# Performance work log

Measured on AMD Instinct MI355X. Metric: run time of the kernel, lower is better.

## Reference

```python
import jax, jax.numpy as jnp
import numpy as np

DIM = 2
WIDTH = 128
N = 262144
T = 101
W0 = 44.0


def setup_inputs() -> dict:
    key = jax.random.key(0)
    ks = jax.random.split(key, 7)
    # time grid: arange scaled to [0, 1] (dt = 0.01)
    t = jnp.arange(T, dtype=jnp.float32) / (T - 1)
    x0 = jax.random.normal(ks[0], (N, DIM), dtype=jnp.float32)
    # SIREN init: first layer U(-1/dim, 1/dim); later layers U(-sqrt(6/fan_in)/w0, +)
    c0 = 1.0 / DIM
    ch = float(np.sqrt(6.0 / WIDTH) / W0)
    W1 = jax.random.uniform(ks[1], (DIM, WIDTH), jnp.float32, -c0, c0)
    b1 = jax.random.uniform(ks[2], (WIDTH,), jnp.float32, -c0, c0)
    W2 = jax.random.uniform(ks[3], (WIDTH, WIDTH), jnp.float32, -ch, ch)
    b2 = jax.random.uniform(ks[4], (WIDTH,), jnp.float32, -ch, ch)
    W3 = jax.random.uniform(ks[5], (WIDTH, DIM), jnp.float32, -ch, ch)
    b3 = jax.random.uniform(ks[6], (DIM,), jnp.float32, -ch, ch)
    return {"t": t, "x0": x0, "W1": W1, "b1": b1, "W2": W2, "b2": b2, "W3": W3, "b3": b3}


def reference(t, x0, W1, b1, W2, b2, W3, b3):
    def f(x):
        h = jnp.sin(W0 * (x @ W1 + b1))   # [N, WIDTH]
        h = jnp.sin(W0 * (h @ W2 + b2))   # [N, WIDTH]
        return h @ W3 + b3                # [N, DIM]

    # torchdiffeq fixed-grid 'rk4' uses the 3/8-rule (rk4_alt_step_func)
    def step(y, dt):
        k1 = f(y)
        k2 = f(y + dt * k1 / 3.0)
        k3 = f(y + dt * (k2 - k1 / 3.0))
        k4 = f(y + dt * (k1 - k2 + k3))
        y1 = y + (k1 + 3.0 * (k2 + k3) + k4) * dt * 0.125
        return y1, y1

    dts = t[1:] - t[:-1]                  # [T-1]
    _, ys = jax.lax.scan(step, x0, dts)   # [T-1, N, DIM]
    return jnp.concatenate([x0[None], ys], axis=0)  # [T, N, DIM]
```

## Files before the change

### kernel.cpp

```cpp
#include <hip/hip_runtime.h>


#define W0F    44.0f
#define INV2PI 0.15915494309189535f
#define SCALE  (W0F * INV2PI)
#define WIDTH  128
#define NPART  262144
#define TSTEPS 101

typedef short s16x8 __attribute__((ext_vector_type(8)));
typedef float f32x4 __attribute__((ext_vector_type(4)));

__device__ __forceinline__ float sin_rev(float z) {
    return __builtin_amdgcn_sinf(z);
}
__device__ __forceinline__ unsigned short f2bf(float x) {
    __bf16 b = (__bf16)x;
    return __builtin_bit_cast(unsigned short, b);
}
__device__ __forceinline__ float bf2f(unsigned short u) {
    unsigned int v = ((unsigned int)u) << 16;
    return __builtin_bit_cast(float, v);
}
__device__ __forceinline__ float trunc16f(float v) {
    return __builtin_bit_cast(float, __builtin_bit_cast(unsigned int, v) & 0xffff0000u);
}
__device__ __forceinline__ unsigned int pack_hi16(float vlo, float vhi) {
    return __builtin_amdgcn_perm(__builtin_bit_cast(unsigned int, vhi),
                                 __builtin_bit_cast(unsigned int, vlo),
                                 0x07060302u);
}

#define ROR_ADD(x, ctrl) ((x) + __builtin_bit_cast(float, \
    __builtin_amdgcn_update_dpp(0, __builtin_bit_cast(int, (x)), (ctrl), 0xF, 0xF, false)))
__device__ __forceinline__ float row_sum16(float x) {
    x = ROR_ADD(x, 0x128);
    x = ROR_ADD(x, 0x124);
    x = ROR_ADD(x, 0x122);
    x = ROR_ADD(x, 0x121);
    return x;
}

__device__ __forceinline__ float sel16(const float g[16], int idx) {
    float a[8], b[4], c[2];
    #pragma unroll
    for (int i = 0; i < 8; ++i) a[i] = (idx & 8) ? g[i + 8] : g[i];
    #pragma unroll
    for (int i = 0; i < 4; ++i) b[i] = (idx & 4) ? a[i + 4] : a[i];
    #pragma unroll
    for (int i = 0; i < 2; ++i) c[i] = (idx & 2) ? b[i + 2] : b[i];
    return (idx & 1) ? c[1] : c[0];
}

__global__ void prep_kernel(const float* __restrict__ W1, const float* __restrict__ b1,
                            const float* __restrict__ W2, float* __restrict__ ws) {
    int i = blockIdx.x * blockDim.x + threadIdx.x;
    unsigned short* whi = (unsigned short*)ws;
    unsigned short* wlo = whi + 16384;
    if (i < 16384) {
        int j = i & 7, l = (i >> 3) & 63, c = (i >> 9) & 3, nt = (i >> 11) & 7;
        int k = 32 * c + 8 * (l >> 4) + j;
        int n = 16 * nt + (l & 15);
        float v = SCALE * W2[k * WIDTH + n];
        unsigned short hi = f2bf(v);
        whi[i] = hi;
        wlo[i] = f2bf(v - bf2f(hi));
    }
    if (i < 2 * WIDTH) ws[16384 + i] = SCALE * W1[i];
    if (i < WIDTH)     ws[16384 + 256 + i] = SCALE * b1[i];
}

__launch_bounds__(256, 2)
__global__ void ode_kernel(const float* __restrict__ t,
                           const float2* __restrict__ x0,
                           const float* __restrict__ ws,
                           const float* __restrict__ W3,
                           const float* __restrict__ b2,
                           const float* __restrict__ b3,
                           float2* __restrict__ out) {
    __shared__ unsigned int sBh[8192];
    __shared__ unsigned int sBl[8192];
    __shared__ __align__(16) float sWx[WIDTH], sWy[WIDTH], sWb[WIDTH];
    __shared__ float2 sW3[WIDTH];
    __shared__ float  sB2[WIDTH];

    const int tid = threadIdx.x;
    const int wave = tid >> 6;
    const int lane = tid & 63;
    const int lane15 = lane & 15;
    const int kg = lane >> 4;

    {
        const uint4* srch = (const uint4*)ws;
        const uint4* srcl = (const uint4*)(ws + 8192);
        uint4* dsth = (uint4*)sBh;
        uint4* dstl = (uint4*)sBl;
        #pragma unroll
        for (int j = 0; j < 8; ++j) {
            dsth[tid + 256 * j] = srch[tid + 256 * j];
            dstl[tid + 256 * j] = srcl[tid + 256 * j];
        }
    }
    if (tid < WIDTH) {
        sWx[tid] = ws[16384 + tid];
        sWy[tid] = ws[16384 + WIDTH + tid];
        sWb[tid] = ws[16384 + 256 + tid];
        sW3[tid] = make_float2(W3[2 * tid], W3[2 * tid + 1]);
        sB2[tid] = SCALE * b2[tid];
    }
    __syncthreads();

    const int mloc = 16 * (lane15 >> 2) + 4 * kg + (lane15 & 3);
    const int p = blockIdx.x * 256 + wave * 64 + mloc;

    float2 y = x0[p];
    out[p] = y;

    const float b30 = b3[0], b31 = b3[1];

    float tprev = t[0];
    #pragma unroll 1
    for (int step = 0; step < TSTEPS - 1; ++step) {
        const float tnext = t[step + 1];
        const float dt = tnext - tprev;
        tprev = tnext;

        float k1x=0.f,k1y=0.f,k2x=0.f,k2y=0.f,k3x=0.f,k3y=0.f,sx=0.f,sy=0.f;

        #pragma unroll 1
        for (int s = 0; s < 4; ++s) {
            float yinx, yiny;
            if (s == 0)      { yinx = y.x;                                 yiny = y.y; }
            else if (s == 1) { const float c1 = dt * (1.0f / 3.0f);
                               yinx = y.x + c1 * k1x;                       yiny = y.y + c1 * k1y; }
            else if (s == 2) { yinx = y.x + dt * (k2x - (1.0f/3.0f) * k1x); yiny = y.y + dt * (k2y - (1.0f/3.0f) * k1y); }
            else             { yinx = y.x + dt * (k1x - k2x + k3x);         yiny = y.y + dt * (k1y - k2y + k3y); }

            float qx[4], qy[4];
            {
                const int sbase = 16 * (lane15 >> 2) + (lane15 & 3);
                qx[0] = __shfl(yinx, sbase,      64); qy[0] = __shfl(yiny, sbase,      64);
                qx[1] = __shfl(yinx, sbase + 4,  64); qy[1] = __shfl(yiny, sbase + 4,  64);
                qx[2] = __shfl(yinx, sbase + 8,  64); qy[2] = __shfl(yiny, sbase + 8,  64);
                qx[3] = __shfl(yinx, sbase + 12, 64); qy[3] = __shfl(yiny, sbase + 12, 64);
            }

            f32x4 acc[8][4];
            #pragma unroll
            for (int i = 0; i < 8; ++i) {
                const float bb = sB2[16 * i + lane15];
                const f32x4 v4 = (f32x4){bb, bb, bb, bb};
                #pragma unroll
                for (int mt = 0; mt < 4; ++mt) acc[i][mt] = v4;
            }

            #pragma unroll 1
            for (int c = 0; c < 4; ++c) {
                uint4 ah[4], al[4];
                #pragma unroll
                for (int jq = 0; jq < 2; ++jq) {
                    float4 wxv = *(const float4*)&sWx[32 * c + 8 * kg + 4 * jq];
                    float4 wyv = *(const float4*)&sWy[32 * c + 8 * kg + 4 * jq];
                    float4 wbv = *(const float4*)&sWb[32 * c + 8 * kg + 4 * jq];
                    #pragma unroll
                    for (int mt = 0; mt < 4; ++mt) {
                        float v0 = sin_rev(fmaf(qx[mt], wxv.x, fmaf(qy[mt], wyv.x, wbv.x)));
                        float v1 = sin_rev(fmaf(qx[mt], wxv.y, fmaf(qy[mt], wyv.y, wbv.y)));
                        float v2 = sin_rev(fmaf(qx[mt], wxv.z, fmaf(qy[mt], wyv.z, wbv.z)));
                        float v3 = sin_rev(fmaf(qx[mt], wxv.w, fmaf(qy[mt], wyv.w, wbv.w)));
                        float r0 = v0 - trunc16f(v0);
                        float r1 = v1 - trunc16f(v1);
                        float r2 = v2 - trunc16f(v2);
                        float r3 = v3 - trunc16f(v3);
                        if (jq == 0) {
                            ah[mt].x = pack_hi16(v0, v1); ah[mt].y = pack_hi16(v2, v3);
                            al[mt].x = pack_hi16(r0, r1); al[mt].y = pack_hi16(r2, r3);
                        } else {
                            ah[mt].z = pack_hi16(v0, v1); ah[mt].w = pack_hi16(v2, v3);
                            al[mt].z = pack_hi16(r0, r1); al[mt].w = pack_hi16(r2, r3);
                        }
                    }
                }

                __builtin_amdgcn_s_setprio(1);
                #pragma unroll
                for (int nt = 0; nt < 8; ++nt) {
                    const int fo = (nt * 4 + c) * 256 + lane * 4;
                    uint4 bhU = *(const uint4*)&sBh[fo];
                    uint4 blU = *(const uint4*)&sBl[fo];
                    s16x8 bh = __builtin_bit_cast(s16x8, bhU);
                    s16x8 bl = __builtin_bit_cast(s16x8, blU);
                    #pragma unroll
                    for (int mt = 0; mt < 4; ++mt) {
                        s16x8 ahv = __builtin_bit_cast(s16x8, ah[mt]);
                        s16x8 alv = __builtin_bit_cast(s16x8, al[mt]);
                        acc[nt][mt] = __builtin_amdgcn_mfma_f32_16x16x32_bf16(ahv, bh, acc[nt][mt], 0, 0, 0);
                        acc[nt][mt] = __builtin_amdgcn_mfma_f32_16x16x32_bf16(alv, bh, acc[nt][mt], 0, 0, 0);
                        acc[nt][mt] = __builtin_amdgcn_mfma_f32_16x16x32_bf16(ahv, bl, acc[nt][mt], 0, 0, 0);
                    }
                }
                __builtin_amdgcn_s_setprio(0);
            }

            float gx[16], gy[16];
            #pragma unroll
            for (int i = 0; i < 16; ++i) { gx[i] = 0.f; gy[i] = 0.f; }
            #pragma unroll
            for (int nt = 0; nt < 8; ++nt) {
                float2 w3v = sW3[16 * nt + lane15];
                #pragma unroll
                for (int mt = 0; mt < 4; ++mt) {
                    #pragma unroll
                    for (int r = 0; r < 4; ++r) {
                        float sn = sin_rev(acc[nt][mt][r]);
                        gx[4*mt+r] = fmaf(sn, w3v.x, gx[4*mt+r]);
                        gy[4*mt+r] = fmaf(sn, w3v.y, gy[4*mt+r]);
                    }
                }
            }
            #pragma unroll
            for (int i = 0; i < 16; ++i) { gx[i] = row_sum16(gx[i]); gy[i] = row_sum16(gy[i]); }
            const float fx = b30 + sel16(gx, lane15);
            const float fy = b31 + sel16(gy, lane15);

            if (s == 0)      { k1x = fx; k1y = fy; sx = fx;        sy = fy; }
            else if (s == 1) { k2x = fx; k2y = fy; sx += 3.f * fx; sy += 3.f * fy; }
            else if (s == 2) { k3x = fx; k3y = fy; sx += 3.f * fx; sy += 3.f * fy; }
            else             {                     sx += fx;       sy += fy; }
        }

        const float cc = dt * 0.125f;
        y.x += sx * cc;
        y.y += sy * cc;
        out[(size_t)(step + 1) * NPART + p] = y;
    }
}

extern "C" void kernel_launch(void* const* d_in, const int* in_sizes, int n_in,
                              void* d_out, int out_size, void* d_ws, size_t ws_size,
                              hipStream_t stream) {
    const float*  t  = (const float*)d_in[0];
    const float2* x0 = (const float2*)d_in[1];
    const float*  W1 = (const float*)d_in[2];
    const float*  b1 = (const float*)d_in[3];
    const float*  W2 = (const float*)d_in[4];
    const float*  b2 = (const float*)d_in[5];
    const float*  W3 = (const float*)d_in[6];
    const float*  b3 = (const float*)d_in[7];
    float* ws = (float*)d_ws;
    float2* out = (float2*)d_out;

    prep_kernel<<<64, 256, 0, stream>>>(W1, b1, W2, ws);
    ode_kernel<<<NPART / 256, 256, 0, stream>>>(t, x0, ws, W3, b2, b3, out);
}
```

Before: 9.494 ms.

## Transpose layer-2 GEMM to 32x32x16 MFMA with particles on the N dimension

Recasts the hidden-layer matmul so W2 becomes the A operand (prep reorders it into 32x32x16 fragments) and the per-particle sine activations become the B operand, using 32x32x16 bf16 MFMAs instead of 16x16x32. Each lane now owns its own particle, so the output projection reduces within the lane and needs only one cross-half shuffle, replacing the DPP row sums and 16-way select. Blocks also rotate their k-slice start by block parity, likely to spread LDS bank access. The larger accumulator tiles keep the register footprint the same but change MFMA latency and issue patterns.

Result: slower. 12.34 ms (+29.9%).

```diff
diff --git a/kernel.cpp b/kernel.cpp
--- a/kernel.cpp
+++ b/kernel.cpp
@@ -8,8 +8,8 @@
 #define NPART  262144
 #define TSTEPS 101
 
-typedef short s16x8 __attribute__((ext_vector_type(8)));
-typedef float f32x4 __attribute__((ext_vector_type(4)));
+typedef short s16x8  __attribute__((ext_vector_type(8)));
+typedef float f32x16 __attribute__((ext_vector_type(16)));
 
 __device__ __forceinline__ float sin_rev(float z) {
     return __builtin_amdgcn_sinf(z);
@@ -29,27 +29,6 @@
     return __builtin_amdgcn_perm(__builtin_bit_cast(unsigned int, vhi),
                                  __builtin_bit_cast(unsigned int, vlo),
                                  0x07060302u);
-}
-
-#define ROR_ADD(x, ctrl) ((x) + __builtin_bit_cast(float, \
-    __builtin_amdgcn_update_dpp(0, __builtin_bit_cast(int, (x)), (ctrl), 0xF, 0xF, false)))
-__device__ __forceinline__ float row_sum16(float x) {
-    x = ROR_ADD(x, 0x128);
-    x = ROR_ADD(x, 0x124);
-    x = ROR_ADD(x, 0x122);
-    x = ROR_ADD(x, 0x121);
-    return x;
-}
-
-__device__ __forceinline__ float sel16(const float g[16], int idx) {
-    float a[8], b[4], c[2];
-    #pragma unroll
-    for (int i = 0; i < 8; ++i) a[i] = (idx & 8) ? g[i + 8] : g[i];
-    #pragma unroll
-    for (int i = 0; i < 4; ++i) b[i] = (idx & 4) ? a[i + 4] : a[i];
-    #pragma unroll
-    for (int i = 0; i < 2; ++i) c[i] = (idx & 2) ? b[i + 2] : b[i];
-    return (idx & 1) ? c[1] : c[0];
 }
 
 __global__ void prep_kernel(const float* __restrict__ W1, const float* __restrict__ b1,
@@ -58,10 +37,10 @@
     unsigned short* whi = (unsigned short*)ws;
     unsigned short* wlo = whi + 16384;
     if (i < 16384) {
-        int j = i & 7, l = (i >> 3) & 63, c = (i >> 9) & 3, nt = (i >> 11) & 7;
-        int k = 32 * c + 8 * (l >> 4) + j;
-        int n = 16 * nt + (l & 15);
-        float v = SCALE * W2[k * WIDTH + n];
+        int j = i & 7, l = (i >> 3) & 63, ks = (i >> 9) & 7, mt = (i >> 12) & 3;
+        int k = 16 * ks + 8 * (l >> 5) + j;
+        int m = 32 * mt + (l & 31);
+        float v = SCALE * W2[k * WIDTH + m];
         unsigned short hi = f2bf(v);
         whi[i] = hi;
         wlo[i] = f2bf(v - bf2f(hi));
@@ -81,14 +60,14 @@
     __shared__ unsigned int sBh[8192];
     __shared__ unsigned int sBl[8192];
     __shared__ __align__(16) float sWx[WIDTH], sWy[WIDTH], sWb[WIDTH];
-    __shared__ float2 sW3[WIDTH];
-    __shared__ float  sB2[WIDTH];
+    __shared__ __align__(16) float2 sW3[WIDTH];
+    __shared__ __align__(16) float  sB2[WIDTH];
 
     const int tid = threadIdx.x;
     const int wave = tid >> 6;
     const int lane = tid & 63;
-    const int lane15 = lane & 15;
-    const int kg = lane >> 4;
+    const int lane31 = lane & 31;
+    const int h5 = lane >> 5;
 
     {
         const uint4* srch = (const uint4*)ws;
@@ -110,13 +89,13 @@
     }
     __syncthreads();
 
-    const int mloc = 16 * (lane15 >> 2) + 4 * kg + (lane15 & 3);
-    const int p = blockIdx.x * 256 + wave * 64 + mloc;
+    const int p = blockIdx.x * 256 + wave * 64 + lane;
 
     float2 y = x0[p];
     out[p] = y;
 
     const float b30 = b3[0], b31 = b3[1];
+    const int ksrot = (blockIdx.x & 1) << 2;
 
     float tprev = t[0];
     #pragma unroll 1
@@ -136,92 +115,107 @@
             else if (s == 2) { yinx = y.x + dt * (k2x - (1.0f/3.0f) * k1x); yiny = y.y + dt * (k2y - (1.0f/3.0f) * k1y); }
             else             { yinx = y.x + dt * (k1x - k2x + k3x);         yiny = y.y + dt * (k1y - k2y + k3y); }
 
-            float qx[4], qy[4];
-            {
-                const int sbase = 16 * (lane15 >> 2) + (lane15 & 3);
-                qx[0] = __shfl(yinx, sbase,      64); qy[0] = __shfl(yiny, sbase,      64);
-                qx[1] = __shfl(yinx, sbase + 4,  64); qy[1] = __shfl(yiny, sbase + 4,  64);
-                qx[2] = __shfl(yinx, sbase + 8,  64); qy[2] = __shfl(yiny, sbase + 8,  64);
-                qx[3] = __shfl(yinx, sbase + 12, 64); qy[3] = __shfl(yiny, sbase + 12, 64);
+            const float qx0 = __shfl(yinx, lane31,      64);
+            const float qy0 = __shfl(yiny, lane31,      64);
+            const float qx1 = __shfl(yinx, lane31 + 32, 64);
+            const float qy1 = __shfl(yiny, lane31 + 32, 64);
+
+            f32x16 acc[4][2];
+            #pragma unroll
+            for (int mt = 0; mt < 4; ++mt) {
+                #pragma unroll
+                for (int g = 0; g < 4; ++g) {
+                    float4 bb = *(const float4*)&sB2[32 * mt + 8 * g + 4 * h5];
+                    acc[mt][0][4*g+0] = bb.x; acc[mt][0][4*g+1] = bb.y;
+                    acc[mt][0][4*g+2] = bb.z; acc[mt][0][4*g+3] = bb.w;
+                    acc[mt][1][4*g+0] = bb.x; acc[mt][1][4*g+1] = bb.y;
+                    acc[mt][1][4*g+2] = bb.z; acc[mt][1][4*g+3] = bb.w;
+                }
             }
 
-            f32x4 acc[8][4];
-            #pragma unroll
-            for (int i = 0; i < 8; ++i) {
-                const float bb = sB2[16 * i + lane15];
-                const f32x4 v4 = (f32x4){bb, bb, bb, bb};
-                #pragma unroll
-                for (int mt = 0; mt < 4; ++mt) acc[i][mt] = v4;
-            }
-
             #pragma unroll 1
-            for (int c = 0; c < 4; ++c) {
-                uint4 ah[4], al[4];
+            for (int kk = 0; kk < 8; ++kk) {
+                const int ks = (kk + ksrot) & 7;
+                uint4 bh0, bh1, bl0, bl1;
                 #pragma unroll
                 for (int jq = 0; jq < 2; ++jq) {
-                    float4 wxv = *(const float4*)&sWx[32 * c + 8 * kg + 4 * jq];
-                    float4 wyv = *(const float4*)&sWy[32 * c + 8 * kg + 4 * jq];
-                    float4 wbv = *(const float4*)&sWb[32 * c + 8 * kg + 4 * jq];
+                    float4 wxv = *(const float4*)&sWx[16 * ks + 8 * h5 + 4 * jq];
+                    float4 wyv = *(const float4*)&sWy[16 * ks + 8 * h5 + 4 * jq];
+                    float4 wbv = *(const float4*)&sWb[16 * ks + 8 * h5 + 4 * jq];
                     #pragma unroll
-                    for (int mt = 0; mt < 4; ++mt) {
-                        float v0 = sin_rev(fmaf(qx[mt], wxv.x, fmaf(qy[mt], wyv.x, wbv.x)));
-                        float v1 = sin_rev(fmaf(qx[mt], wxv.y, fmaf(qy[mt], wyv.y, wbv.y)));
-                        float v2 = sin_rev(fmaf(qx[mt], wxv.z, fmaf(qy[mt], wyv.z, wbv.z)));
-                        float v3 = sin_rev(fmaf(qx[mt], wxv.w, fmaf(qy[mt], wyv.w, wbv.w)));
+                    for (int n = 0; n < 2; ++n) {
+                        const float qxm = n ? qx1 : qx0;
+                        const float qym = n ? qy1 : qy0;
+                        float v0 = sin_rev(fmaf(qxm, wxv.x, fmaf(qym, wyv.x, wbv.x)));
+                        float v1 = sin_rev(fmaf(qxm, wxv.y, fmaf(qym, wyv.y, wbv.y)));
+                        float v2 = sin_rev(fmaf(qxm, wxv.z, fmaf(qym, wyv.z, wbv.z)));
+                        float v3 = sin_rev(fmaf(qxm, wxv.w, fmaf(qym, wyv.w, wbv.w)));
                         float r0 = v0 - trunc16f(v0);
                         float r1 = v1 - trunc16f(v1);
                         float r2 = v2 - trunc16f(v2);
                         float r3 = v3 - trunc16f(v3);
-                        if (jq == 0) {
-                            ah[mt].x = pack_hi16(v0, v1); ah[mt].y = pack_hi16(v2, v3);
-                            al[mt].x = pack_hi16(r0, r1); al[mt].y = pack_hi16(r2, r3);
+                        unsigned int hA = pack_hi16(v0, v1), hB = pack_hi16(v2, v3);
+                        unsigned int lA = pack_hi16(r0, r1), lB = pack_hi16(r2, r3);
+                        if (n == 0) {
+                            if (jq == 0) { bh0.x = hA; bh0.y = hB; bl0.x = lA; bl0.y = lB; }
+                            else         { bh0.z = hA; bh0.w = hB; bl0.z = lA; bl0.w = lB; }
                         } else {
-                            ah[mt].z = pack_hi16(v0, v1); ah[mt].w = pack_hi16(v2, v3);
-                            al[mt].z = pack_hi16(r0, r1); al[mt].w = pack_hi16(r2, r3);
+                            if (jq == 0) { bh1.x = hA; bh1.y = hB; bl1.x = lA; bl1.y = lB; }
+                            else         { bh1.z = hA; bh1.w = hB; bl1.z = lA; bl1.w = lB; }
                         }
                     }
                 }
+                s16x8 vbh0 = __builtin_bit_cast(s16x8, bh0);
+                s16x8 vbh1 = __builtin_bit_cast(s16x8, bh1);
+                s16x8 vbl0 = __builtin_bit_cast(s16x8, bl0);
+                s16x8 vbl1 = __builtin_bit_cast(s16x8, bl1);
 
                 __builtin_amdgcn_s_setprio(1);
                 #pragma unroll
-                for (int nt = 0; nt < 8; ++nt) {
-                    const int fo = (nt * 4 + c) * 256 + lane * 4;
-                    uint4 bhU = *(const uint4*)&sBh[fo];
-                    uint4 blU = *(const uint4*)&sBl[fo];
-                    s16x8 bh = __builtin_bit_cast(s16x8, bhU);
-                    s16x8 bl = __builtin_bit_cast(s16x8, blU);
-                    #pragma unroll
-                    for (int mt = 0; mt < 4; ++mt) {
-                        s16x8 ahv = __builtin_bit_cast(s16x8, ah[mt]);
-                        s16x8 alv = __builtin_bit_cast(s16x8, al[mt]);
-                        acc[nt][mt] = __builtin_amdgcn_mfma_f32_16x16x32_bf16(ahv, bh, acc[nt][mt], 0, 0, 0);
-                        acc[nt][mt] = __builtin_amdgcn_mfma_f32_16x16x32_bf16(alv, bh, acc[nt][mt], 0, 0, 0);
-                        acc[nt][mt] = __builtin_amdgcn_mfma_f32_16x16x32_bf16(ahv, bl, acc[nt][mt], 0, 0, 0);
-                    }
+                for (int mt = 0; mt < 4; ++mt) {
+                    const int fo = (mt * 8 + ks) * 256 + lane * 4;
+                    uint4 ahU = *(const uint4*)&sBh[fo];
+                    uint4 alU = *(const uint4*)&sBl[fo];
+                    s16x8 ah = __builtin_bit_cast(s16x8, ahU);
+                    s16x8 al = __builtin_bit_cast(s16x8, alU);
+                    acc[mt][0] = __builtin_amdgcn_mfma_f32_32x32x16_bf16(ah, vbh0, acc[mt][0], 0, 0, 0);
+                    acc[mt][0] = __builtin_amdgcn_mfma_f32_32x32x16_bf16(al, vbh0, acc[mt][0], 0, 0, 0);
+                    acc[mt][0] = __builtin_amdgcn_mfma_f32_32x32x16_bf16(ah, vbl0, acc[mt][0], 0, 0, 0);
+                    acc[mt][1] = __builtin_amdgcn_mfma_f32_32x32x16_bf16(ah, vbh1, acc[mt][1], 0, 0, 0);
+                    acc[mt][1] = __builtin_amdgcn_mfma_f32_32x32x16_bf16(al, vbh1, acc[mt][1], 0, 0, 0);
+                    acc[mt][1] = __builtin_amdgcn_mfma_f32_32x32x16_bf16(ah, vbl1, acc[mt][1], 0, 0, 0);
                 }
                 __builtin_amdgcn_s_setprio(0);
             }
 
-            float gx[16], gy[16];
+            float px0[2] = {0.f, 0.f}, py0[2] = {0.f, 0.f};
+            float px1[2] = {0.f, 0.f}, py1[2] = {0.f, 0.f};
             #pragma unroll
-            for (int i = 0; i < 16; ++i) { gx[i] = 0.f; gy[i] = 0.f; }
-            #pragma unroll
-            for (int nt = 0; nt < 8; ++nt) {
-                float2 w3v = sW3[16 * nt + lane15];
-                #pragma unroll
-                for (int mt = 0; mt < 4; ++mt) {
+            for (int mt = 0; mt < 4; ++mt) {
+                #pragma unroll
+                for (int g = 0; g < 4; ++g) {
+                    const float4* w3p = (const float4*)&sW3[32 * mt + 8 * g + 4 * h5];
+                    float4 wA = w3p[0];
+                    float4 wB = w3p[1];
                     #pragma unroll
-                    for (int r = 0; r < 4; ++r) {
-                        float sn = sin_rev(acc[nt][mt][r]);
-                        gx[4*mt+r] = fmaf(sn, w3v.x, gx[4*mt+r]);
-                        gy[4*mt+r] = fmaf(sn, w3v.y, gy[4*mt+r]);
+                    for (int q = 0; q < 4; ++q) {
+                        const float w3x = (q == 0) ? wA.x : (q == 1) ? wA.z : (q == 2) ? wB.x : wB.z;
+                        const float w3y = (q == 0) ? wA.y : (q == 1) ? wA.w : (q == 2) ? wB.y : wB.w;
+                        float s0 = sin_rev(acc[mt][0][4*g+q]);
+                        float s1 = sin_rev(acc[mt][1][4*g+q]);
+                        px0[g & 1] = fmaf(s0, w3x, px0[g & 1]);
+                        py0[g & 1] = fmaf(s0, w3y, py0[g & 1]);
+                        px1[g & 1] = fmaf(s1, w3x, px1[g & 1]);
+                        py1[g & 1] = fmaf(s1, w3y, py1[g & 1]);
                     }
                 }
             }
-            #pragma unroll
-            for (int i = 0; i < 16; ++i) { gx[i] = row_sum16(gx[i]); gy[i] = row_sum16(gy[i]); }
-            const float fx = b30 + sel16(gx, lane15);
-            const float fy = b31 + sel16(gy, lane15);
+            const float gx0 = px0[0] + px0[1], gy0 = py0[0] + py0[1];
+            const float gx1 = px1[0] + px1[1], gy1 = py1[0] + py1[1];
+            const float ownx = h5 ? gx1 : gx0, sndx = h5 ? gx0 : gx1;
+            const float owny = h5 ? gy1 : gy0, sndy = h5 ? gy0 : gy1;
+            const float fx = b30 + ownx + __shfl_xor(sndx, 32, 64);
+            const float fy = b31 + owny + __shfl_xor(sndy, 32, 64);
 
             if (s == 0)      { k1x = fx; k1y = fy; sx = fx;        sy = fy; }
             else if (s == 1) { k2x = fx; k2y = fy; sx += 3.f * fx; sy += 3.f * fy; }
```
